# Optimization experiments

Measured on AMD Instinct MI355X. Metric: run time of the kernel, lower is better.

Reference implementation:

```python
import jax, jax.numpy as jnp
import numpy as np

B, P, M, C = 8, 131072, 16, 2
THRESHOLD = 0.5
GAMMA = 2.0
ALPHA_W = 0.25  # focal 'weight' for the foreground class


def _cxcycz_to_xyz(b):
    return jnp.concatenate([b[..., :3] - b[..., 3:] / 2, b[..., :3] + b[..., 3:] / 2], -1)


def _xyz_to_cxcycz(b):
    return jnp.concatenate([(b[..., :3] + b[..., 3:]) / 2, b[..., 3:] - b[..., :3]], -1)


def _encode(cxcycz, priors_cxcycz):
    # standard SSD encoding with variances (10, 5), extended to 3D
    return jnp.concatenate([
        (cxcycz[..., :3] - priors_cxcycz[..., :3]) / (priors_cxcycz[..., 3:] / 10.0),
        jnp.log(cxcycz[..., 3:] / priors_cxcycz[..., 3:]) * 5.0], -1)


def _jaccard3d(a, b):
    # a: [M,6] xyz boxes, b: [P,6] xyz boxes -> [M,P] IoU
    lo = jnp.maximum(a[:, None, :3], b[None, :, :3])
    hi = jnp.minimum(a[:, None, 3:], b[None, :, 3:])
    inter = jnp.prod(jnp.clip(hi - lo, 0.0, None), -1)
    va = jnp.prod(a[:, 3:] - a[:, :3], -1)
    vb = jnp.prod(b[:, 3:] - b[:, :3], -1)
    return inter / (va[:, None] + vb[None, :] - inter)


def setup_inputs():
    key = jax.random.key(0)
    k1, k2, k3, k4, k5, k6 = jax.random.split(key, 6)
    predicted_locs = jax.random.normal(k1, (B, P, 6), jnp.float32)
    predicted_scores = jax.random.normal(k2, (B, P, C), jnp.float32)
    # valid ground-truth boxes in boundary (xyz) coords inside unit cube
    ctr = jax.random.uniform(k3, (B, M, 3)) * 0.8 + 0.1
    sz = jax.random.uniform(k4, (B, M, 3)) * 0.15 + 0.05
    boxes = jnp.concatenate([ctr - sz / 2, ctr + sz / 2], -1)
    # priors in center-size (cxcycz) coords
    pctr = jax.random.uniform(k5, (P, 3)) * 0.9 + 0.05
    psz = jax.random.uniform(k6, (P, 3)) * 0.2 + 0.03
    priors_cxcycz = jnp.concatenate([pctr, psz], -1)
    labels = jnp.ones((B, M), jnp.int32)  # single foreground class
    return dict(predicted_locs=predicted_locs, predicted_scores=predicted_scores,
                boxes=boxes, labels=labels, priors_cxcycz=priors_cxcycz)


def _forward(predicted_locs, predicted_scores, boxes, priors_cxcycz, labels):
    priors_xyz = _cxcycz_to_xyz(priors_cxcycz)

    def match(boxes_i, labels_i):
        ov = _jaccard3d(boxes_i, priors_xyz)           # [M, P]
        overlap_fep = ov.max(0)                        # [P] best IoU per prior
        object_fep = ov.argmax(0)                      # [P] best object per prior
        prior_feo = ov.argmax(1)                       # [M] best prior per object
        # force each object to own its best prior
        object_fep = object_fep.at[prior_feo].set(jnp.arange(M))
        overlap_fep = overlap_fep.at[prior_feo].set(1.0)
        lab = labels_i[object_fep]
        lab = jnp.where(overlap_fep < THRESHOLD, 0, lab)  # hard thresholding
        tl = _encode(_xyz_to_cxcycz(boxes_i[object_fep]), priors_cxcycz)
        return lab, tl

    true_classes, true_locs = jax.vmap(match)(boxes, labels)  # [B,P], [B,P,6]

    pos = true_classes > 0
    n_pos = pos.sum()
    # nn.L1Loss() = mean over all selected elements (n_pos priors x 6 coords)
    diff = jnp.abs(predicted_locs - true_locs) * pos[..., None].astype(predicted_locs.dtype)
    loc_loss = jnp.where(n_pos > 0,
                         diff.sum() / jnp.maximum(n_pos.astype(jnp.float32) * 6.0, 1.0),
                         jnp.float32(0.0))

    # sigmoid focal loss on foreground channel (include_background=False, C==2)
    x = predicted_scores[..., 1]                       # [B,P] fg logit
    t = pos.astype(x.dtype)
    ce = -(t * jax.nn.log_sigmoid(x) + (1.0 - t) * jax.nn.log_sigmoid(-x))
    p = jax.nn.sigmoid(x)
    pt = jnp.where(pos, p, 1.0 - p)
    focal = (ALPHA_W * t + (1.0 - ALPHA_W) * (1.0 - t)) * (1.0 - pt) ** GAMMA * ce
    conf_loss = focal.mean()
    return conf_loss, loc_loss


def reference(predicted_locs, predicted_scores, boxes, labels, priors_cxcycz):
    return _forward(predicted_locs, predicted_scores, boxes, priors_cxcycz, labels)
```

## Files before the change

### kernel.cpp

```cpp
#include <hip/hip_runtime.h>

#define NB 8
#define NP 131072
#define NM 16
#define THRESH 0.5f
#define BLK 256
#define PPT 2
#define PPB (BLK * PPT)
#define BPB (NP / PPB)
#define MATCH_BLOCKS (NB * BPB)
#define FOCAL_BLOCKS 128
#define NBLOCKS (MATCH_BLOCKS + FOCAL_BLOCKS)
#define NPAIR (NB * NM)

typedef unsigned long long u64;
typedef unsigned int u32;


template <int CTRL>
__device__ __forceinline__ float dppmv(float x) {
    return __int_as_float(__builtin_amdgcn_update_dpp(
        0, __float_as_int(x), CTRL, 0xf, 0xf, false));
}

__device__ __forceinline__ float wave_max63(float x) {
    x = fmaxf(x, dppmv<0x111>(x));
    x = fmaxf(x, dppmv<0x112>(x));
    x = fmaxf(x, dppmv<0x114>(x));
    x = fmaxf(x, dppmv<0x118>(x));
    x = fmaxf(x, dppmv<0x142>(x));
    x = fmaxf(x, dppmv<0x143>(x));
    return x;
}

__device__ __forceinline__ float wave_sum63(float x) {
    x += dppmv<0x111>(x);
    x += dppmv<0x112>(x);
    x += dppmv<0x114>(x);
    x += dppmv<0x118>(x);
    x += dppmv<0x142>(x);
    x += dppmv<0x143>(x);
    return x;
}

__device__ __forceinline__ float bcast63(float x) {
    return __int_as_float(__builtin_amdgcn_readlane(__float_as_int(x), 63));
}


__device__ __forceinline__ float iou_term(float inter, float va, float vb) {
    return (inter > 0.0f) ? inter * __builtin_amdgcn_rcpf(va + vb - inter) : 0.0f;
}

__device__ __forceinline__ float focal_term(float x, bool pos) {
    float t = __expf(-fabsf(x));
    float r = __builtin_amdgcn_rcpf(1.0f + t);
    float L = __logf(1.0f + t);
    float ce = (pos ? fmaxf(-x, 0.0f) : fmaxf(x, 0.0f)) + L;
    float omp = (pos == (x >= 0.0f)) ? t * r : r;
    float w = pos ? 0.25f : 0.75f;
    return w * omp * omp * ce;
}

__device__ __forceinline__ float l1_enc(const float* lp,
                                        const float blo[3], const float bhi[3],
                                        const float pc[3], const float ps[3]) {
    float s = 0.0f;
#pragma unroll
    for (int k = 0; k < 3; ++k) {
        float gc = (blo[k] + bhi[k]) / 2.0f;
        float gs = bhi[k] - blo[k];
        float e  = (gc - pc[k]) / (ps[k] / 10.0f);
        float e2 = __logf(gs / ps[k]) * 5.0f;
        s += fabsf(lp[k]     - e);
        s += fabsf(lp[3 + k] - e2);
    }
    return s;
}

__device__ __forceinline__ u32 decode_p(u64 k) { return ~(u32)(k & 0xFFFFFFFFull); }


__global__ __launch_bounds__(BLK) void main_kernel(
        const float* __restrict__ locs, const float* __restrict__ scores,
        const float* __restrict__ boxes, const int* __restrict__ labels,
        const float* __restrict__ priors,
        u64* __restrict__ keys_out,
        float4* __restrict__ part) {
    __shared__ float4 s_box[NM][2];
    __shared__ u64    s_wkey[4][NM];
    __shared__ float  s_wred[4][3];

    const int tid  = threadIdx.x;
    const int bid  = blockIdx.x;
    const int lane = tid & 63, wave = tid >> 6;

    if (bid >= MATCH_BLOCKS) {
        const int fblk = bid - MATCH_BLOCKS;
        const float4* sc4 = reinterpret_cast<const float4*>(scores);
        float f = 0.0f;
#pragma unroll
        for (int i = 0; i < 16; ++i) {
            float4 v = sc4[(size_t)fblk * 4096 + i * BLK + tid];
            f += focal_term(v.y, false) + focal_term(v.w, false);
        }
        f = wave_sum63(f);
        if (lane == 63) s_wred[wave][0] = f;
        __syncthreads();
        if (tid == 0)
            part[bid] = make_float4(s_wred[0][0] + s_wred[1][0] +
                                    s_wred[2][0] + s_wred[3][0], 0.0f, 0.0f, 0.0f);
        return;
    }

    const int b    = bid >> 8;
    const int xblk = bid & (BPB - 1);
    const int p0   = (xblk << 9) + 2 * tid;
    const int pbase = (xblk << 9) + (wave << 7);

    if (tid < NM) {
        const float* bx = &boxes[(b * NM + tid) * 6];
        float l0 = bx[0], l1 = bx[1], l2 = bx[2];
        float h0 = bx[3], h1 = bx[4], h2 = bx[5];
        s_box[tid][0] = make_float4(l0, l1, l2, h0);
        float va = (h0 - l0) * (h1 - l1) * (h2 - l2);
        s_box[tid][1] = make_float4(h1, h2, va, __int_as_float(labels[b * NM + tid]));
    }
    __syncthreads();

    const float4* pr4 = reinterpret_cast<const float4*>(priors);
    const size_t f4b = (size_t)(p0 / 2) * 3;
    float pl0[3], ph0[3], pl1[3], ph1[3];
    float vb0, vb1;
    {
        float4 q0 = pr4[f4b + 0], q1 = pr4[f4b + 1], q2 = pr4[f4b + 2];
        const float pc0[3] = {q0.x, q0.y, q0.z}, ps0[3] = {q0.w, q1.x, q1.y};
        const float pc1[3] = {q1.z, q1.w, q2.x}, ps1[3] = {q2.y, q2.z, q2.w};
#pragma unroll
        for (int k = 0; k < 3; ++k) {
            pl0[k] = pc0[k] - ps0[k] / 2.0f; ph0[k] = pc0[k] + ps0[k] / 2.0f;
            pl1[k] = pc1[k] - ps1[k] / 2.0f; ph1[k] = pc1[k] + ps1[k] / 2.0f;
        }
        vb0 = (ph0[0] - pl0[0]) * (ph0[1] - pl0[1]) * (ph0[2] - pl0[2]);
        vb1 = (ph1[0] - pl1[0]) * (ph1[1] - pl1[1]) * (ph1[2] - pl1[2]);
    }

    float ci[NM];
    u32 spack = 0u;
    float best0 = -1.0f, best1 = -1.0f;
    int bm0 = 0, bm1 = 0;
#pragma unroll
    for (int m = 0; m < NM; ++m) {
        float4 A = s_box[m][0], B4 = s_box[m][1];
        float d0 = fminf(A.w,  ph0[0]) - fmaxf(A.x, pl0[0]);
        float d1 = fminf(B4.x, ph0[1]) - fmaxf(A.y, pl0[1]);
        float d2 = fminf(B4.y, ph0[2]) - fmaxf(A.z, pl0[2]);
        float i0 = iou_term(fmaxf(d0, 0.0f) * fmaxf(d1, 0.0f) * fmaxf(d2, 0.0f),
                            B4.z, vb0);
        d0 = fminf(A.w,  ph1[0]) - fmaxf(A.x, pl1[0]);
        d1 = fminf(B4.x, ph1[1]) - fmaxf(A.y, pl1[1]);
        d2 = fminf(B4.y, ph1[2]) - fmaxf(A.z, pl1[2]);
        float i1 = iou_term(fmaxf(d0, 0.0f) * fmaxf(d1, 0.0f) * fmaxf(d2, 0.0f),
                            B4.z, vb1);
        if (i0 > best0) { best0 = i0; bm0 = m; }
        if (i1 > best1) { best1 = i1; bm1 = m; }
        const bool s1 = (i1 > i0);
        ci[m] = s1 ? i1 : i0;
        spack |= (s1 ? 1u : 0u) << m;
    }

#pragma unroll
    for (int m = 0; m < NM; ++m) {
        float wm = bcast63(wave_max63(ci[m]));
        u64 eq = __ballot(ci[m] == wm);
        int ls = __ffsll(eq) - 1;
        u32 sp = (u32)__builtin_amdgcn_readlane((int)spack, ls);
        u32 wp = (u32)(pbase + 2 * ls) + ((sp >> m) & 1u);
        if (lane == 0)
            s_wkey[wave][m] = ((u64)__float_as_uint(wm) << 32) | (u32)~wp;
    }

    float f = 0.0f, l = 0.0f, n = 0.0f;
    {
        float4 Bb = s_box[bm0][1];
        if ((best0 >= THRESH) && (__float_as_int(Bb.w) > 0)) {
            const float x = scores[((size_t)b * NP + p0) * 2 + 1];
            f += focal_term(x, true) - focal_term(x, false);
            float4 Ab = s_box[bm0][0];
            float blo[3] = {Ab.x, Ab.y, Ab.z}, bhi[3] = {Ab.w, Bb.x, Bb.y};
            float pc[3], ps[3];
#pragma unroll
            for (int k = 0; k < 3; ++k) { pc[k] = priors[p0 * 6 + k]; ps[k] = priors[p0 * 6 + 3 + k]; }
            l += l1_enc(&locs[((size_t)b * NP + p0) * 6], blo, bhi, pc, ps);
            n += 1.0f;
        }
        Bb = s_box[bm1][1];
        if ((best1 >= THRESH) && (__float_as_int(Bb.w) > 0)) {
            const int p1 = p0 + 1;
            const float x = scores[((size_t)b * NP + p1) * 2 + 1];
            f += focal_term(x, true) - focal_term(x, false);
            float4 Ab = s_box[bm1][0];
            float blo[3] = {Ab.x, Ab.y, Ab.z}, bhi[3] = {Ab.w, Bb.x, Bb.y};
            float pc[3], ps[3];
#pragma unroll
            for (int k = 0; k < 3; ++k) { pc[k] = priors[p1 * 6 + k]; ps[k] = priors[p1 * 6 + 3 + k]; }
            l += l1_enc(&locs[((size_t)b * NP + p1) * 6], blo, bhi, pc, ps);
            n += 1.0f;
        }
    }

    f = wave_sum63(f); l = wave_sum63(l); n = wave_sum63(n);
    if (lane == 63) { s_wred[wave][0] = f; s_wred[wave][1] = l; s_wred[wave][2] = n; }
    __syncthreads();

    if (tid < NM) {
        u64 k = s_wkey[0][tid];
#pragma unroll
        for (int w = 1; w < 4; ++w) k = (s_wkey[w][tid] > k) ? s_wkey[w][tid] : k;
        keys_out[(size_t)(b * NM + tid) * BPB + xblk] = k;
    }
    if (tid == 0) {
        part[bid] = make_float4(s_wred[0][0] + s_wred[1][0] + s_wred[2][0] + s_wred[3][0],
                                s_wred[0][1] + s_wred[1][1] + s_wred[2][1] + s_wred[3][1],
                                s_wred[0][2] + s_wred[1][2] + s_wred[2][2] + s_wred[3][2],
                                0.0f);
    }
}


__global__ __launch_bounds__(1024) void finalize_kernel(
        const float* __restrict__ locs, const float* __restrict__ scores,
        const float* __restrict__ boxes, const int* __restrict__ labels,
        const float* __restrict__ priors, const u64* __restrict__ keys_in,
        const float4* __restrict__ part, float* __restrict__ out) {
    __shared__ u64   s_key[NPAIR];
    __shared__ float s_red[16][3];
    __shared__ float s_fix[16][3];
    const int t = threadIdx.x, lane = t & 63, wave = t >> 6;

    float f = 0.0f, l = 0.0f, n = 0.0f;
    for (int i = t; i < NBLOCKS; i += 1024) {
        float4 v = part[i]; f += v.x; l += v.y; n += v.z;
    }
    f = wave_sum63(f); l = wave_sum63(l); n = wave_sum63(n);
    if (lane == 63) { s_red[wave][0] = f; s_red[wave][1] = l; s_red[wave][2] = n; }

#pragma unroll
    for (int i = 0; i < 8; ++i) {
        const int pair = wave * 8 + i;
        const u64* kp = keys_in + (size_t)pair * BPB;
        u64 k = 0;
#pragma unroll
        for (int j = 0; j < BPB / 64; ++j) {
            u64 v = kp[j * 64 + lane];
            k = (v > k) ? v : k;
        }
#pragma unroll
        for (int off = 32; off > 0; off >>= 1) {
            u64 o = __shfl_down(k, off);
            k = (o > k) ? o : k;
        }
        if (lane == 0) s_key[pair] = k;
    }
    __syncthreads();

    float df = 0.0f, dl = 0.0f, dn = 0.0f;
    if (t < NPAIR) {
        const int b = t / NM, m = t % NM;
        const u32 pstar = decode_p(s_key[t]);
        bool skip = false;
        for (int mm = m + 1; mm < NM; ++mm)
            skip |= (decode_p(s_key[b * NM + mm]) == pstar);
        if (!skip) {
            const int p = (int)pstar;
            float pc[3], ps[3], pl[3], ph[3];
#pragma unroll
            for (int k = 0; k < 3; ++k) { pc[k] = priors[p * 6 + k]; ps[k] = priors[p * 6 + 3 + k]; }
#pragma unroll
            for (int k = 0; k < 3; ++k) { pl[k] = pc[k] - ps[k] / 2.0f; ph[k] = pc[k] + ps[k] / 2.0f; }
            const float vb = (ph[0] - pl[0]) * (ph[1] - pl[1]) * (ph[2] - pl[2]);

            float best = -1.0f; int bestm = 0;
            for (int mm = 0; mm < NM; ++mm) {
                const float* bx = &boxes[(b * NM + mm) * 6];
                float d0 = fminf(bx[3], ph[0]) - fmaxf(bx[0], pl[0]);
                float d1 = fminf(bx[4], ph[1]) - fmaxf(bx[1], pl[1]);
                float d2 = fminf(bx[5], ph[2]) - fmaxf(bx[2], pl[2]);
                float inter = fmaxf(d0, 0.0f) * fmaxf(d1, 0.0f) * fmaxf(d2, 0.0f);
                float va = (bx[3] - bx[0]) * (bx[4] - bx[1]) * (bx[5] - bx[2]);
                float iou = iou_term(inter, va, vb);
                if (iou > best) { best = iou; bestm = mm; }
            }
            const bool old_pos = (best >= THRESH) && (labels[b * NM + bestm] > 0);
            const bool new_pos = (labels[b * NM + m] > 0);

            const float x = scores[((size_t)b * NP + p) * 2 + 1];
            df = focal_term(x, new_pos) - focal_term(x, old_pos);
            dn = (new_pos ? 1.0f : 0.0f) - (old_pos ? 1.0f : 0.0f);

            const float* lp = &locs[((size_t)b * NP + p) * 6];
            if (new_pos) {
                const float* bx = &boxes[(b * NM + m) * 6];
                float blo[3] = {bx[0], bx[1], bx[2]}, bhi[3] = {bx[3], bx[4], bx[5]};
                dl += l1_enc(lp, blo, bhi, pc, ps);
            }
            if (old_pos) {
                const float* bx = &boxes[(b * NM + bestm) * 6];
                float blo[3] = {bx[0], bx[1], bx[2]}, bhi[3] = {bx[3], bx[4], bx[5]};
                dl -= l1_enc(lp, blo, bhi, pc, ps);
            }
        }
    }
    df = wave_sum63(df); dl = wave_sum63(dl); dn = wave_sum63(dn);
    if (lane == 63) { s_fix[wave][0] = df; s_fix[wave][1] = dl; s_fix[wave][2] = dn; }
    __syncthreads();

    if (t == 0) {
        float tf = 0.0f, tl = 0.0f, tn = 0.0f;
        for (int w = 0; w < 16; ++w) {
            tf += s_red[w][0] + s_fix[w][0];
            tl += s_red[w][1] + s_fix[w][1];
            tn += s_red[w][2] + s_fix[w][2];
        }
        out[0] = tf / (float)(NB * NP);
        out[1] = (tn > 0.5f) ? tl / fmaxf(tn * 6.0f, 1.0f) : 0.0f;
    }
}


extern "C" void kernel_launch(void* const* d_in, const int* in_sizes, int n_in,
                              void* d_out, int out_size, void* d_ws, size_t ws_size,
                              hipStream_t stream) {
    const float* locs   = (const float*)d_in[0];
    const float* scores = (const float*)d_in[1];
    const float* boxes  = (const float*)d_in[2];
    const int*   labels = (const int*)d_in[3];
    const float* priors = (const float*)d_in[4];
    float* out = (float*)d_out;

    u64*    keys = (u64*)d_ws;
    float4* part = (float4*)((char*)d_ws + (size_t)NPAIR * BPB * 8);

    main_kernel<<<NBLOCKS, BLK, 0, stream>>>(locs, scores, boxes, labels, priors,
                                             keys, part);
    finalize_kernel<<<1, 1024, 0, stream>>>(locs, scores, boxes, labels, priors, keys,
                                            part, out);
}
```

Measured before the change: 36.32 us.

## Fuse per-box wave reductions into IoU loop and reorder focal blocks first

Moves the per-box wave max/ballot reduction into the IoU loop and disables unrolling, so the 16-entry ci array and packed select bits are no longer held. This cuts register pressure to raise occupancy. The focal-only blocks are now placed at the start of the grid, and the focal loop is no longer unrolled. Prior centre and size are rebuilt from the lo/hi corners already in registers instead of being reloaded from global memory, at the cost of slight float rounding differences and a serialized loop with less ILP.

```diff
diff --git a/kernel.cpp b/kernel.cpp
--- a/kernel.cpp
+++ b/kernel.cpp
@@ -95,13 +95,11 @@
     const int bid  = blockIdx.x;
     const int lane = tid & 63, wave = tid >> 6;
 
-    if (bid >= MATCH_BLOCKS) {
-        const int fblk = bid - MATCH_BLOCKS;
+    if (bid < FOCAL_BLOCKS) {
         const float4* sc4 = reinterpret_cast<const float4*>(scores);
         float f = 0.0f;
-#pragma unroll
         for (int i = 0; i < 16; ++i) {
-            float4 v = sc4[(size_t)fblk * 4096 + i * BLK + tid];
+            float4 v = sc4[(size_t)bid * 4096 + i * BLK + tid];
             f += focal_term(v.y, false) + focal_term(v.w, false);
         }
         f = wave_sum63(f);
@@ -113,8 +111,9 @@
         return;
     }
 
-    const int b    = bid >> 8;
-    const int xblk = bid & (BPB - 1);
+    const int mbid = bid - FOCAL_BLOCKS;
+    const int b    = mbid >> 8;
+    const int xblk = mbid & (BPB - 1);
     const int p0   = (xblk << 9) + 2 * tid;
     const int pbase = (xblk << 9) + (wave << 7);
 
@@ -128,11 +127,10 @@
     }
     __syncthreads();
 
-    const float4* pr4 = reinterpret_cast<const float4*>(priors);
-    const size_t f4b = (size_t)(p0 / 2) * 3;
-    float pl0[3], ph0[3], pl1[3], ph1[3];
-    float vb0, vb1;
+    float pl0[3], ph0[3], pl1[3], ph1[3], vb0, vb1;
     {
+        const float4* pr4 = reinterpret_cast<const float4*>(priors);
+        const size_t f4b = (size_t)(p0 / 2) * 3;
         float4 q0 = pr4[f4b + 0], q1 = pr4[f4b + 1], q2 = pr4[f4b + 2];
         const float pc0[3] = {q0.x, q0.y, q0.z}, ps0[3] = {q0.w, q1.x, q1.y};
         const float pc1[3] = {q1.z, q1.w, q2.x}, ps1[3] = {q2.y, q2.z, q2.w};
@@ -145,11 +143,9 @@
         vb1 = (ph1[0] - pl1[0]) * (ph1[1] - pl1[1]) * (ph1[2] - pl1[2]);
     }
 
-    float ci[NM];
-    u32 spack = 0u;
     float best0 = -1.0f, best1 = -1.0f;
     int bm0 = 0, bm1 = 0;
-#pragma unroll
+#pragma unroll 1
     for (int m = 0; m < NM; ++m) {
         float4 A = s_box[m][0], B4 = s_box[m][1];
         float d0 = fminf(A.w,  ph0[0]) - fmaxf(A.x, pl0[0]);
@@ -164,20 +160,16 @@
                             B4.z, vb1);
         if (i0 > best0) { best0 = i0; bm0 = m; }
         if (i1 > best1) { best1 = i1; bm1 = m; }
+
         const bool s1 = (i1 > i0);
-        ci[m] = s1 ? i1 : i0;
-        spack |= (s1 ? 1u : 0u) << m;
-    }
-
-#pragma unroll
-    for (int m = 0; m < NM; ++m) {
-        float wm = bcast63(wave_max63(ci[m]));
-        u64 eq = __ballot(ci[m] == wm);
+        float v = s1 ? i1 : i0;
+        float wm = bcast63(wave_max63(v));
+        u64 eq = __ballot(v == wm);
         int ls = __ffsll(eq) - 1;
-        u32 sp = (u32)__builtin_amdgcn_readlane((int)spack, ls);
-        u32 wp = (u32)(pbase + 2 * ls) + ((sp >> m) & 1u);
+        u32 sl = (u32)__builtin_amdgcn_readlane((int)(s1 ? 1 : 0), ls);
         if (lane == 0)
-            s_wkey[wave][m] = ((u64)__float_as_uint(wm) << 32) | (u32)~wp;
+            s_wkey[wave][m] = ((u64)__float_as_uint(wm) << 32)
+                            | (u32)~(u32)((u32)(pbase + 2 * ls) + sl);
     }
 
     float f = 0.0f, l = 0.0f, n = 0.0f;
@@ -188,23 +180,22 @@
             f += focal_term(x, true) - focal_term(x, false);
             float4 Ab = s_box[bm0][0];
             float blo[3] = {Ab.x, Ab.y, Ab.z}, bhi[3] = {Ab.w, Bb.x, Bb.y};
-            float pc[3], ps[3];
-#pragma unroll
-            for (int k = 0; k < 3; ++k) { pc[k] = priors[p0 * 6 + k]; ps[k] = priors[p0 * 6 + 3 + k]; }
+            const float pc[3] = {(pl0[0] + ph0[0]) / 2.0f, (pl0[1] + ph0[1]) / 2.0f,
+                                 (pl0[2] + ph0[2]) / 2.0f};
+            const float ps[3] = {ph0[0] - pl0[0], ph0[1] - pl0[1], ph0[2] - pl0[2]};
             l += l1_enc(&locs[((size_t)b * NP + p0) * 6], blo, bhi, pc, ps);
             n += 1.0f;
         }
         Bb = s_box[bm1][1];
         if ((best1 >= THRESH) && (__float_as_int(Bb.w) > 0)) {
-            const int p1 = p0 + 1;
-            const float x = scores[((size_t)b * NP + p1) * 2 + 1];
+            const float x = scores[((size_t)b * NP + p0 + 1) * 2 + 1];
             f += focal_term(x, true) - focal_term(x, false);
             float4 Ab = s_box[bm1][0];
             float blo[3] = {Ab.x, Ab.y, Ab.z}, bhi[3] = {Ab.w, Bb.x, Bb.y};
-            float pc[3], ps[3];
-#pragma unroll
-            for (int k = 0; k < 3; ++k) { pc[k] = priors[p1 * 6 + k]; ps[k] = priors[p1 * 6 + 3 + k]; }
-            l += l1_enc(&locs[((size_t)b * NP + p1) * 6], blo, bhi, pc, ps);
+            const float pc[3] = {(pl1[0] + ph1[0]) / 2.0f, (pl1[1] + ph1[1]) / 2.0f,
+                                 (pl1[2] + ph1[2]) / 2.0f};
+            const float ps[3] = {ph1[0] - pl1[0], ph1[1] - pl1[1], ph1[2] - pl1[2]};
+            l += l1_enc(&locs[((size_t)b * NP + p0 + 1) * 6], blo, bhi, pc, ps);
             n += 1.0f;
         }
     }
```

Result: slower. 38.30 us (+5.5%).
